# Kernel tuning notes

Hardware: AMD Instinct MI355X
Metric: run time of the kernel (lower is better)

Reference implementation:

```python
import jax, jax.numpy as jnp
import numpy as np
from jax import lax

B, T, C, H, N = 4, 1024, 2048, 32, 64
KVH = 8            # kv heads -> kv_dim = 512, n_rep = 4
GN_EPS = 0.00064   # group_norm eps from Step3


def _l2norm(x):
    # torch F.normalize(p=2, dim=-1) with eps=1e-12
    n = jnp.linalg.norm(x, axis=-1, keepdims=True)
    return x / jnp.maximum(n, 1e-12)


def _rwkv7_scan(r, decay, k, v, aa, bb, state):
    # all inputs (B,T,H,N); state (B,H,N,N) with layout [value, key]
    def step(S, inp):
        r_t, d_t, k_t, v_t, a_t, b_t = inp  # each (B,H,N)
        sa = jnp.einsum('bhik,bhk->bhi', S, a_t)
        S = (S * d_t[:, :, None, :]
             + sa[..., None] * b_t[:, :, None, :]
             + v_t[..., None] * k_t[:, :, None, :])
        y = jnp.einsum('bhik,bhk->bhi', S, r_t)
        return S, y
    xs = tuple(jnp.moveaxis(t, 1, 0) for t in (r, decay, k, v, aa, bb))  # (T,B,H,N)
    state, ys = lax.scan(step, state, xs)
    return jnp.moveaxis(ys, 0, 1), state  # (B,T,H,N), (B,H,N,N)


def _forward(x, v_first, state, R, R_bias, K, K_bias, V, V_bias, O, O_bias,
             w0, w1, w2, a0, a1, a2, v0, v1, v2, k_k, k_a, r_k, ln_w, ln_b):
    # ---- Step1: projections + gates (hybrid_matmul -> plain matmul in fp32 ref) ----
    r = x @ R.T + R_bias                                   # (B,T,C)
    w_raw = -jax.nn.softplus(-(w0 + jnp.tanh(x @ w1) @ w2)) - 0.6
    k = x @ K.T + K_bias                                   # (B,T,512)
    v = x @ V.T + V_bias
    n_rep = C // K.shape[0]
    k = jnp.repeat(k.reshape(B, T, KVH, N), n_rep, axis=2).reshape(B, T, C)
    v = jnp.repeat(v.reshape(B, T, KVH, N), n_rep, axis=2).reshape(B, T, C)
    a = jax.nn.sigmoid(a0 + (x @ a1) @ a2)
    kk = _l2norm((k * k_k).reshape(B, T, H, N)).reshape(B, T, C)
    k = k * (1.0 + (a - 1.0) * k_a)
    # layer_id != 0: cross-layer value blending
    v = v + (v_first - v) * jax.nn.sigmoid(v0 + (x @ v1) @ v2)
    aa = -kk
    bb = kk * a
    # ---- Step2: fused recurrent rwkv7 (fp32 state) ----
    decay = jnp.exp(-jnp.exp(w_raw.astype(jnp.float32)))
    rs = lambda t: t.astype(jnp.float32).reshape(B, T, H, N)
    y, state_out = _rwkv7_scan(rs(r), decay.reshape(B, T, H, N), rs(k), rs(v), rs(aa), rs(bb), state)
    # ---- Step3: group norm over (T, N) per (batch, head) as in the (B,C,T) permute ----
    mean = y.mean(axis=(1, 3), keepdims=True)
    var = ((y - mean) ** 2).mean(axis=(1, 3), keepdims=True)
    yn = (y - mean) * lax.rsqrt(var + GN_EPS)
    xx = (yn * ln_w.reshape(H, N) + ln_b.reshape(H, N)).reshape(B, T, C)
    bonus = ((r.reshape(B, T, H, N) * k.reshape(B, T, H, N) * r_k.reshape(H, N))
             .sum(-1, keepdims=True) * v.reshape(B, T, H, N)).reshape(B, T, C)
    xx = xx + bonus
    out = xx @ O.T + O_bias
    return out


def setup_inputs() -> dict:
    key = jax.random.key(0)
    ks = jax.random.split(key, 25)
    g = lambda i, shape, s: jax.random.normal(ks[i], shape, dtype=jnp.float32) * s
    return {
        'x': g(0, (B, T, C), 1.0),
        'v_first': g(1, (B, T, C), 1.0),
        'state': jnp.zeros((B, H, N, N), dtype=jnp.float32),
        'R': g(2, (C, C), 0.02), 'R_bias': jnp.zeros((C,), jnp.float32),
        'K': g(3, (KVH * N, C), 0.02), 'K_bias': jnp.zeros((KVH * N,), jnp.float32),
        'V': g(4, (KVH * N, C), 0.02), 'V_bias': jnp.zeros((KVH * N,), jnp.float32),
        'O': g(5, (C, C), 0.02), 'O_bias': jnp.zeros((C,), jnp.float32),
        'w0': g(6, (C,), 0.1), 'w1': g(7, (C, 64), 0.05), 'w2': g(8, (64, C), 0.05),
        'a0': g(9, (C,), 0.1), 'a1': g(10, (C, 64), 0.05), 'a2': g(11, (64, C), 0.05),
        'v0': g(12, (C,), 0.1), 'v1': g(13, (C, 32), 0.05), 'v2': g(14, (32, C), 0.05),
        'k_k': 1.0 + g(15, (C,), 0.05),
        'k_a': 1.0 + g(16, (C,), 0.05),
        'r_k': g(17, (C,), 0.1),
        'ln_w': jnp.ones((C,), jnp.float32),
        'ln_b': jnp.zeros((C,), jnp.float32),
    }


def reference(x, v_first, state, R, R_bias, K, K_bias, V, V_bias, O, O_bias,
              w0, w1, w2, a0, a1, a2, v0, v1, v2, k_k, k_a, r_k, ln_w, ln_b):
    return _forward(x, v_first, state, R, R_bias, K, K_bias, V, V_bias, O, O_bias,
                    w0, w1, w2, a0, a1, a2, v0, v1, v2, k_k, k_a, r_k, ln_w, ln_b)
```

## Files before the change

### kernel.cpp

```cpp
#include <hip/hip_runtime.h>
#include <hip/hip_bf16.h>
#include <math.h>

typedef __attribute__((ext_vector_type(8))) short bf16x8;
typedef __attribute__((ext_vector_type(4))) float f32x4;

__device__ __forceinline__ unsigned short f2b(float f) {
  unsigned u = __float_as_uint(f);
  unsigned r = (u + 0x7FFF + ((u >> 16) & 1)) >> 16;
  return (unsigned short)r;
}

__device__ __forceinline__ void async16(const void* g, void* l) {
  __builtin_amdgcn_global_load_lds(
      (const __attribute__((address_space(1))) unsigned int*)(g),
      (__attribute__((address_space(3))) unsigned int*)(l), 16, 0, 0);
}

__device__ __forceinline__ float rowsum16(float x) {
  x += __int_as_float(__builtin_amdgcn_update_dpp(0, __float_as_int(x), 0x121, 0xF, 0xF, false));
  x += __int_as_float(__builtin_amdgcn_update_dpp(0, __float_as_int(x), 0x122, 0xF, 0xF, false));
  x += __int_as_float(__builtin_amdgcn_update_dpp(0, __float_as_int(x), 0x124, 0xF, 0xF, false));
  x += __int_as_float(__builtin_amdgcn_update_dpp(0, __float_as_int(x), 0x128, 0xF, 0xF, false));
  return x;
}

__device__ __forceinline__ float mixhi(float a, unsigned pk, float c) {
  float d;
  asm("v_fma_mix_f32 %0, %1, %2, %3 op_sel:[0,1,0] op_sel_hi:[0,1,0]"
      : "=v"(d) : "v"(a), "v"(pk), "v"(c));
  return d;
}
__device__ __forceinline__ float mixlo(float a, unsigned pk, float c) {
  float d;
  asm("v_fma_mix_f32 %0, %1, %2, %3 op_sel:[0,0,0] op_sel_hi:[0,1,0]"
      : "=v"(d) : "v"(a), "v"(pk), "v"(c));
  return d;
}
__device__ __forceinline__ float h2f(unsigned h) {
  float f; asm("v_cvt_f32_f16 %0, %1" : "=v"(f) : "v"(h)); return f;
}

__global__ __launch_bounds__(256) void cvt4_kernel(
    const float* __restrict__ x, const float* __restrict__ R,
    const float* __restrict__ K, const float* __restrict__ V,
    const float* __restrict__ Ow,
    unsigned short* __restrict__ xb, unsigned short* __restrict__ RKVb,
    unsigned short* __restrict__ Ob)
{
  const int bid = blockIdx.x;
  const float* s; unsigned short* d; int i;
  if (bid < 8192)       { s = x; d = xb; i = bid * 256 + threadIdx.x; }
  else if (bid < 12288) { s = R; d = RKVb; i = (bid - 8192) * 256 + threadIdx.x; }
  else if (bid < 13312) { s = K; d = RKVb + 2048 * 2048; i = (bid - 12288) * 256 + threadIdx.x; }
  else if (bid < 14336) { s = V; d = RKVb + 2560 * 2048; i = (bid - 13312) * 256 + threadIdx.x; }
  else                  { s = Ow; d = Ob; i = (bid - 14336) * 256 + threadIdx.x; }
  float4 v = ((const float4*)s)[i];
  ushort4 o;
  o.x = f2b(v.x); o.y = f2b(v.y); o.z = f2b(v.z); o.w = f2b(v.w);
  ((ushort4*)d)[i] = o;
}

__global__ __launch_bounds__(256) void tcvt_all(
    const float* __restrict__ w1, const float* __restrict__ a1,
    const float* __restrict__ v1, const float* __restrict__ w2,
    const float* __restrict__ a2, const float* __restrict__ v2,
    unsigned short* __restrict__ Bcat, unsigned short* __restrict__ w2t,
    unsigned short* __restrict__ a2t, unsigned short* __restrict__ v2t)
{
  const int r = blockIdx.x >> 5, i = blockIdx.x & 31;
  const float* in; unsigned short* out; int Kd, Nd, ors, bx, by;
  switch (r) {
    case 0:  in = w1; out = Bcat;             Kd = 2048; Nd = 64;   ors = 2048; bx = 0; by = i; break;
    case 1:  in = a1; out = Bcat + 64 * 2048; Kd = 2048; Nd = 64;   ors = 2048; bx = 0; by = i; break;
    case 2:  in = v1; out = Bcat + 128 * 2048; Kd = 2048; Nd = 32;  ors = 2048; bx = 0; by = i; break;
    case 3:  in = w2; out = w2t;              Kd = 64;   Nd = 2048; ors = 64;   bx = i; by = 0; break;
    case 4:  in = a2; out = a2t;              Kd = 64;   Nd = 2048; ors = 64;   bx = i; by = 0; break;
    default: in = v2; out = v2t;              Kd = 32;   Nd = 2048; ors = 32;   bx = i; by = 0; break;
  }
  __shared__ unsigned short tile[64][65];
  const int tx = threadIdx.x & 63, ty = threadIdx.x >> 6;
  const int n0 = bx * 64, k0 = by * 64;
  #pragma unroll
  for (int j = 0; j < 16; ++j) {
    const int k = k0 + j * 4 + ty;
    const int n = n0 + tx;
    unsigned short v = 0;
    if (k < Kd && n < Nd) v = f2b(in[(size_t)k * Nd + n]);
    tile[j * 4 + ty][tx] = v;
  }
  __syncthreads();
  #pragma unroll
  for (int j = 0; j < 16; ++j) {
    const int n = n0 + j * 4 + ty;
    const int k = k0 + tx;
    if (n < Nd && k < Kd) out[(size_t)n * ors + k] = tile[tx][j * 4 + ty];
  }
}

template<int OUTBF16, int ACT>
__device__ __forceinline__ void gemm_body(
    const unsigned short* __restrict__ A, int lda,
    const unsigned short* __restrict__ B, int ldb,
    const float* __restrict__ bias, void* __restrict__ Cv, int ldc,
    int M, int N, int K, int row0, int col0)
{
  __shared__ __align__(16) unsigned short As[128 * 32];
  __shared__ __align__(16) unsigned short Bs[128 * 32];
  const int tid = threadIdx.x;
  const int w = tid >> 6, lane = tid & 63;
  const int wr = (w >> 1) * 64, wc = (w & 1) * 64;

  f32x4 acc[4][4];
  #pragma unroll
  for (int i = 0; i < 4; ++i)
    #pragma unroll
    for (int j = 0; j < 4; ++j)
      acc[i][j] = (f32x4){0.f, 0.f, 0.f, 0.f};

  const int srow = w * 32 + (lane >> 2);
  const int scol = (lane & 3) * 8;
  const int brow0 = (col0 + srow < N) ? (col0 + srow) : 0;
  const int brow1 = (col0 + srow + 16 < N) ? (col0 + srow + 16) : 0;
  const unsigned short* gA0 = A + (size_t)(row0 + srow) * lda + scol;
  const unsigned short* gA1 = gA0 + (size_t)16 * lda;
  const unsigned short* gB0 = B + (size_t)brow0 * ldb + scol;
  const unsigned short* gB1 = B + (size_t)brow1 * ldb + scol;
  unsigned short* lA0 = As + w * 1024;
  unsigned short* lA1 = As + w * 1024 + 512;
  unsigned short* lB0 = Bs + w * 1024;
  unsigned short* lB1 = Bs + w * 1024 + 512;

  const int m16 = lane & 15;
  const int q8  = (lane >> 4) * 8;

  for (int k0 = 0; k0 < K; k0 += 32) {
    async16(gA0, lA0);
    async16(gA1, lA1);
    async16(gB0, lB0);
    async16(gB1, lB1);
    gA0 += 32; gA1 += 32; gB0 += 32; gB1 += 32;
    __syncthreads();
    bf16x8 af[4], bfr[4];
    #pragma unroll
    for (int i = 0; i < 4; ++i) {
      af[i]  = *(const bf16x8*)(As + (wr + i * 16 + m16) * 32 + q8);
      bfr[i] = *(const bf16x8*)(Bs + (wc + i * 16 + m16) * 32 + q8);
    }
    #pragma unroll
    for (int i = 0; i < 4; ++i)
      #pragma unroll
      for (int j = 0; j < 4; ++j)
        acc[i][j] = __builtin_amdgcn_mfma_f32_16x16x32_bf16(af[i], bfr[j], acc[i][j], 0, 0, 0);
    __syncthreads();
  }

  #pragma unroll
  for (int j = 0; j < 4; ++j) {
    const int c_ = col0 + wc + j * 16 + (lane & 15);
    if (c_ < N) {
      const float bv = bias ? bias[c_] : 0.f;
      #pragma unroll
      for (int i = 0; i < 4; ++i) {
        const int r_ = row0 + wr + i * 16 + (lane >> 4) * 4;
        #pragma unroll
        for (int t4 = 0; t4 < 4; ++t4) {
          float v = acc[i][j][t4] + bv;
          if (ACT == 2 && c_ < 64) v = tanhf(v);
          if (OUTBF16)
            ((unsigned short*)Cv)[(size_t)(r_ + t4) * ldc + c_] = f2b(v);
          else
            ((float*)Cv)[(size_t)(r_ + t4) * ldc + c_] = v;
        }
      }
    }
  }
}

template<int OUTBF16, int ACT>
__global__ __launch_bounds__(256) void gemm_mfma(
    const unsigned short* __restrict__ A, int lda,
    const unsigned short* __restrict__ B, int ldb,
    const float* __restrict__ bias, void* __restrict__ Cv, int ldc,
    int M, int N, int K)
{
  gemm_body<OUTBF16, ACT>(A, lda, B, ldb, bias, Cv, ldc, M, N, K,
                          blockIdx.y * 128, blockIdx.x * 128);
}

__global__ __launch_bounds__(256) void gemm_lr2(
    const unsigned short* __restrict__ hcat,
    const unsigned short* __restrict__ w2t,
    const unsigned short* __restrict__ a2t,
    const unsigned short* __restrict__ v2t,
    float* __restrict__ wt, float* __restrict__ at, float* __restrict__ vt)
{
  const int z = blockIdx.z;
  const unsigned short* A; const unsigned short* Bm; float* C; int K;
  if (z == 0)      { A = hcat;       Bm = w2t; C = wt; K = 64; }
  else if (z == 1) { A = hcat + 64;  Bm = a2t; C = at; K = 64; }
  else             { A = hcat + 128; Bm = v2t; C = vt; K = 32; }
  gemm_body<0, 0>(A, 160, Bm, K, nullptr, C, 2048, 4096, 2048, K,
                  blockIdx.y * 128, blockIdx.x * 128);
}

__global__ __launch_bounds__(256) void gemm_rkvh(
    const unsigned short* __restrict__ A, const unsigned short* __restrict__ B,
    const float* __restrict__ Rb_, const float* __restrict__ Kb_,
    const float* __restrict__ Vb_,
    float* __restrict__ Cr, float* __restrict__ Ck, float* __restrict__ Cvv,
    unsigned short* __restrict__ hcat)
{
  const int col0 = blockIdx.x * 128;
  const int row0 = blockIdx.y * 128;
  float* Cf = nullptr; unsigned short* Ch = nullptr;
  int ldc, cbase; const float* bias = nullptr;
  if (col0 < 2048)      { Cf = Cr;  ldc = 2048; cbase = col0;        bias = Rb_; }
  else if (col0 < 2560) { Cf = Ck;  ldc = 512;  cbase = col0 - 2048; bias = Kb_; }
  else if (col0 < 3072) { Cf = Cvv; ldc = 512;  cbase = col0 - 2560; bias = Vb_; }
  else                  { Ch = hcat; ldc = 160; cbase = col0 - 3072; }

  __shared__ __align__(16) unsigned short As[128 * 32];
  __shared__ __align__(16) unsigned short Bs[128 * 32];
  const int tid = threadIdx.x;
  const int w = tid >> 6, lane = tid & 63;
  const int wr = (w >> 1) * 64, wc = (w & 1) * 64;

  f32x4 acc[4][4];
  #pragma unroll
  for (int i = 0; i < 4; ++i)
    #pragma unroll
    for (int j = 0; j < 4; ++j)
      acc[i][j] = (f32x4){0.f, 0.f, 0.f, 0.f};

  const int srow = w * 32 + (lane >> 2);
  const int scol = (lane & 3) * 8;
  const int brow0 = (col0 + srow < 3232) ? (col0 + srow) : 0;
  const int brow1 = (col0 + srow + 16 < 3232) ? (col0 + srow + 16) : 0;
  const unsigned short* gA0 = A + (size_t)(row0 + srow) * 2048 + scol;
  const unsigned short* gA1 = gA0 + (size_t)16 * 2048;
  const unsigned short* gB0 = B + (size_t)brow0 * 2048 + scol;
  const unsigned short* gB1 = B + (size_t)brow1 * 2048 + scol;
  unsigned short* lA0 = As + w * 1024;
  unsigned short* lA1 = As + w * 1024 + 512;
  unsigned short* lB0 = Bs + w * 1024;
  unsigned short* lB1 = Bs + w * 1024 + 512;

  const int m16 = lane & 15;
  const int q8  = (lane >> 4) * 8;

  for (int k0 = 0; k0 < 2048; k0 += 32) {
    async16(gA0, lA0);
    async16(gA1, lA1);
    async16(gB0, lB0);
    async16(gB1, lB1);
    gA0 += 32; gA1 += 32; gB0 += 32; gB1 += 32;
    __syncthreads();
    bf16x8 af[4], bfr[4];
    #pragma unroll
    for (int i = 0; i < 4; ++i) {
      af[i]  = *(const bf16x8*)(As + (wr + i * 16 + m16) * 32 + q8);
      bfr[i] = *(const bf16x8*)(Bs + (wc + i * 16 + m16) * 32 + q8);
    }
    #pragma unroll
    for (int i = 0; i < 4; ++i)
      #pragma unroll
      for (int j = 0; j < 4; ++j)
        acc[i][j] = __builtin_amdgcn_mfma_f32_16x16x32_bf16(af[i], bfr[j], acc[i][j], 0, 0, 0);
    __syncthreads();
  }

  #pragma unroll
  for (int j = 0; j < 4; ++j) {
    const int c_ = cbase + wc + j * 16 + (lane & 15);
    if (Ch) {
      if (c_ < 160) {
        #pragma unroll
        for (int i = 0; i < 4; ++i) {
          const int r_ = row0 + wr + i * 16 + (lane >> 4) * 4;
          #pragma unroll
          for (int t4 = 0; t4 < 4; ++t4) {
            float v = acc[i][j][t4];
            if (c_ < 64) v = tanhf(v);
            Ch[(size_t)(r_ + t4) * 160 + c_] = f2b(v);
          }
        }
      }
    } else {
      const float bv = bias[c_];
      #pragma unroll
      for (int i = 0; i < 4; ++i) {
        const int r_ = row0 + wr + i * 16 + (lane >> 4) * 4;
        #pragma unroll
        for (int t4 = 0; t4 < 4; ++t4)
          Cf[(size_t)(r_ + t4) * ldc + c_] = acc[i][j][t4] + bv;
      }
    }
  }
}

__global__ __launch_bounds__(256) void prep_kernel(
    const float* __restrict__ k_buf, const float* __restrict__ v_buf,
    const float* __restrict__ r_buf,
    float* wt_decay, const float* __restrict__ at, float* vt_vf,
    const float* __restrict__ v_first,
    const float* __restrict__ w0, const float* __restrict__ a0,
    const float* __restrict__ v0, const float* __restrict__ k_k,
    const float* __restrict__ k_a,
    unsigned* __restrict__ rk_pk, unsigned* __restrict__ ab_pk)
{
  const int row = blockIdx.x;
  const int tid = threadIdx.x;
  const int c0 = tid << 3;
  const int h = tid >> 3;
  const int kvoff = (h >> 2) << 6;
  const size_t base = (size_t)row * 2048;
  const size_t kvrow = (size_t)row * 512;
  float kr[8], kkr[8];
  float ss = 0.f;
  #pragma unroll
  for (int e = 0; e < 8; ++e) {
    const int c = c0 + e;
    const float kv = k_buf[kvrow + kvoff + (c & 63)];
    kr[e] = kv;
    const float t = kv * k_k[c];
    kkr[e] = t;
    ss = fmaf(t, t, ss);
  }
  ss += __shfl_xor(ss, 1);
  ss += __shfl_xor(ss, 2);
  ss += __shfl_xor(ss, 4);
  const float inv = 1.f / fmaxf(sqrtf(ss), 1e-12f);
  #pragma unroll
  for (int e = 0; e < 8; ++e) {
    const int c = c0 + e;
    const size_t idx = base + c;
    const float kk = kkr[e] * inv;
    const float a = 1.f / (1.f + expf(-(a0[c] + at[idx])));
    const float u = w0[c] + wt_decay[idx];
    const float sig_u = 1.f / (1.f + expf(-u));
    wt_decay[idx] = expf(-0.5488116360940264f * sig_u);
    const float kfin = kr[e] * fmaf(a - 1.f, k_a[c], 1.f);
    const float vr = v_buf[kvrow + kvoff + (c & 63)];
    const float sv = 1.f / (1.f + expf(-(v0[c] + vt_vf[idx])));
    vt_vf[idx] = vr + (v_first[idx] - vr) * sv;
    const float bbv = kk * a;
    const float aav = -kk;
    unsigned rk_u, ab_u;
    asm("v_cvt_pkrtz_f16_f32 %0, %1, %2" : "=v"(rk_u) : "v"(r_buf[idx]), "v"(kfin));
    asm("v_cvt_pkrtz_f16_f32 %0, %1, %2" : "=v"(ab_u) : "v"(bbv), "v"(aav));
    rk_pk[idx] = rk_u;
    ab_pk[idx] = ab_u;
  }
}

#define WB(n) asm volatile("s_waitcnt vmcnt(" #n ") lgkmcnt(0)\n\ts_barrier" ::: "memory")
#define BAR2() asm volatile("s_waitcnt lgkmcnt(0)\n\ts_barrier" ::: "memory")

__global__ __launch_bounds__(256) void scan_kernel(
    const unsigned* __restrict__ rkB, const unsigned* __restrict__ abB,
    const float* __restrict__ dB, const float* __restrict__ vB,
    const float* __restrict__ state, float* __restrict__ y,
    float* __restrict__ part)
{
  __shared__ float lds[13824];
  unsigned* ldsU = (unsigned*)lds;
  const int tid = threadIdx.x;
  const int bid = blockIdx.x;
  const int xcd = bid & 7, bj = bid >> 3;
  const int m = bj & 3, gq = bj >> 2;
  const int bh = (gq << 3) | xcd;
  const int widx = tid >> 6;
  const int lane = tid & 63;
  const int rg = lane >> 4;
  const int colg = lane & 15;
  const int rowb = (widx << 2) + rg;
  const int row = (m << 4) + rowb;
  const int b = bh >> 5, h = bh & 31;

  float4 S = *(const float4*)(state + (size_t)bh * 4096 + row * 64 + (colg << 2));

  const unsigned cb = (unsigned)((b * 1024) * 2048 + h * 64);
  const unsigned srow8 = (unsigned)((widx << 3) + rg);
  const unsigned scol = (unsigned)(colg << 2);
  const unsigned sseg = (unsigned)(widx << 9);

  float sacc = 0.f, ssacc = 0.f;
  const float fzero = 0.0f;

  #define STAGE(step0, bofs) do {                                            \
    const unsigned go0_ = cb + ((step0) + srow8) * 2048u + scol;             \
    const unsigned go1_ = go0_ + 4u * 2048u;                                 \
    async16(rkB + go0_, ldsU + (bofs) + sseg);                               \
    async16(rkB + go1_, ldsU + (bofs) + sseg + 256);                         \
    async16(abB + go0_, ldsU + (bofs) + 2048 + sseg);                        \
    async16(abB + go1_, ldsU + (bofs) + 2048 + sseg + 256);                  \
    async16(dB + go0_,  lds + (bofs) + 4096 + sseg);                         \
    async16(dB + go1_,  lds + (bofs) + 4096 + sseg + 256);                   \
    if (lane < 32) {                                                         \
      const unsigned gv_ = cb + ((step0) + (unsigned)(widx << 3)             \
                                 + (unsigned)(lane >> 2)) * 2048u            \
                           + (unsigned)(m << 4) + (unsigned)((lane & 3) << 2); \
      async16(vB + gv_, lds + (bofs) + 6144 + (widx << 7));                  \
    }                                                                        \
  } while (0)

  #define LDRK(bofs, s) (*(const uint4*)(ldsU + (bofs) + (s) * 64 + (colg << 2)))
  #define LDAB(bofs, s) (*(const uint4*)(ldsU + (bofs) + 2048 + (s) * 64 + (colg << 2)))
  #define LDD(bofs, s)  (*(const float4*)(lds + (bofs) + 4096 + (s) * 64 + (colg << 2)))
  #define LDV(bofs, s)  (lds[(bofs) + 6144 + ((s) << 4) + rowb])

  #define PROCESS(bofs) do {                                                 \
    uint4 rk0 = LDRK(bofs, 0), ab0 = LDAB(bofs, 0);                          \
    float4 dv0 = LDD(bofs, 0); float vv0 = LDV(bofs, 0);                     \
    uint4 rk1 = LDRK(bofs, 1), ab1 = LDAB(bofs, 1);                          \
    float4 dv1 = LDD(bofs, 1); float vv1 = LDV(bofs, 1);                     \
    _Pragma("unroll")                                                        \
    for (int s = 0; s < 32; ++s) {                                           \
      const bool ev = ((s & 1) == 0);                                        \
      const uint4 rkc = ev ? rk0 : rk1;                                      \
      const uint4 abc = ev ? ab0 : ab1;                                      \
      const float4 dvc = ev ? dv0 : dv1;                                     \
      const float vvc = ev ? vv0 : vv1;                                      \
      if (s < 30) {                                                          \
        if (ev) {                                                            \
          rk0 = LDRK(bofs, s + 2); ab0 = LDAB(bofs, s + 2);                  \
          dv0 = LDD(bofs, s + 2);  vv0 = LDV(bofs, s + 2);                   \
        } else {                                                             \
          rk1 = LDRK(bofs, s + 2); ab1 = LDAB(bofs, s + 2);                  \
          dv1 = LDD(bofs, s + 2);  vv1 = LDV(bofs, s + 2);                   \
        }                                                                    \
      }                                                                      \
      float t0 = mixhi(S.x, abc.x, fzero);                                   \
      t0 = mixhi(S.y, abc.y, t0);                                            \
      t0 = mixhi(S.z, abc.z, t0);                                            \
      t0 = mixhi(S.w, abc.w, t0);                                            \
      const float sa = rowsum16(t0);                                         \
      float p0 = mixhi(vvc, rkc.x, fzero);                                   \
      float p1 = mixhi(vvc, rkc.y, fzero);                                   \
      float p2 = mixhi(vvc, rkc.z, fzero);                                   \
      float p3 = mixhi(vvc, rkc.w, fzero);                                   \
      p0 = mixlo(sa, abc.x, p0);                                             \
      p1 = mixlo(sa, abc.y, p1);                                             \
      p2 = mixlo(sa, abc.z, p2);                                             \
      p3 = mixlo(sa, abc.w, p3);                                             \
      S.x = fmaf(S.x, dvc.x, p0);                                            \
      S.y = fmaf(S.y, dvc.y, p1);                                            \
      S.z = fmaf(S.z, dvc.z, p2);                                            \
      S.w = fmaf(S.w, dvc.w, p3);                                            \
      float t1 = mixlo(S.x, rkc.x, fzero);                                   \
      t1 = mixlo(S.y, rkc.y, t1);                                            \
      t1 = mixlo(S.z, rkc.z, t1);                                            \
      t1 = mixlo(S.w, rkc.w, t1);                                            \
      const float yv = rowsum16(t1);                                         \
      if (colg == 0) {                                                       \
        lds[13312 + (s << 4) + rowb] = yv;                                   \
        sacc += yv;                                                          \
        ssacc = fmaf(yv, yv, ssacc);                                         \
      }                                                                      \
    }                                                                        \
  } while (0)

  #define YSTORE(step0) do {                                                 \
    const float y0_ = lds[13312 + tid];                                      \
    const float y1_ = lds[13312 + 256 + tid];                                \
    y[cb + ((step0) + (unsigned)(tid >> 4)) * 2048u +                        \
      (unsigned)(m << 4) + (unsigned)(tid & 15)] = y0_;                      \
    y[cb + ((step0) + 16u + (unsigned)(tid >> 4)) * 2048u +                  \
      (unsigned)(m << 4) + (unsigned)(tid & 15)] = y1_;                      \
  } while (0)

  STAGE(0u, 0);
  STAGE(32u, 6656);

  WB(7);
  PROCESS(0);
  BAR2();
  YSTORE(0u);
  STAGE(64u, 0);

  for (int c = 1; c <= 30; ++c) {
    const int bofs = (c & 1) ? 6656 : 0;
    WB(9);
    PROCESS(bofs);
    BAR2();
    YSTORE((unsigned)(c << 5));
    if (c < 30) STAGE((unsigned)((c + 2) << 5), bofs);
  }

  WB(2);
  PROCESS(6656);
  BAR2();
  YSTORE(992u);

  sacc  += __shfl_xor(sacc, 16);
  sacc  += __shfl_xor(sacc, 32);
  ssacc += __shfl_xor(ssacc, 16);
  ssacc += __shfl_xor(ssacc, 32);
  __syncthreads();
  if (lane == 0) { lds[widx] = sacc; lds[4 + widx] = ssacc; }
  __syncthreads();
  if (tid == 0) {
    const float s_  = lds[0] + lds[1] + lds[2] + lds[3];
    const float ss_ = lds[4] + lds[5] + lds[6] + lds[7];
    ((float2*)part)[(bh << 2) + m] = make_float2(s_, ss_);
  }

  #undef STAGE
  #undef PROCESS
  #undef YSTORE
  #undef LDRK
  #undef LDAB
  #undef LDD
  #undef LDV
}

__global__ __launch_bounds__(256) void gapply_kernel(
    const float* __restrict__ y, const unsigned* __restrict__ rkB,
    const float* __restrict__ vf,
    const float* __restrict__ part, const float* __restrict__ r_k,
    const float* __restrict__ ln_w, const float* __restrict__ ln_b,
    unsigned short* __restrict__ xxb)
{
  const int row = blockIdx.x;
  const int b = row >> 10;
  const int tid = threadIdx.x;
  const int h = tid >> 3;
  const int bh = b * 32 + h;
  float s = 0.f, ss = 0.f;
  #pragma unroll
  for (int j = 0; j < 4; ++j) {
    const float2 pr = ((const float2*)part)[(bh << 2) + j];
    s += pr.x; ss += pr.y;
  }
  const float mean = s * (1.f / 65536.f);
  const float rstd = rsqrtf(ss * (1.f / 65536.f) - mean * mean + 0.00064f);
  const int c0 = tid << 3;
  const size_t base = (size_t)row * 2048 + c0;
  float yv[8], vv[8];
  float p = 0.f;
  #pragma unroll
  for (int e = 0; e < 8; ++e) {
    yv[e] = y[base + e];
    vv[e] = vf[base + e];
    const unsigned w_ = rkB[base + e];
    p = fmaf(h2f(w_ & 0xffffu) * h2f(w_ >> 16), r_k[c0 + e], p);
  }
  p += __shfl_xor(p, 1);
  p += __shfl_xor(p, 2);
  p += __shfl_xor(p, 4);
  #pragma unroll
  for (int e = 0; e < 8; ++e) {
    const float yn = (yv[e] - mean) * rstd;
    xxb[base + e] = f2b(fmaf(yn, ln_w[c0 + e], ln_b[c0 + e]) + p * vv[e]);
  }
}

extern "C" void kernel_launch(void* const* d_in, const int* in_sizes, int n_in,
                              void* d_out, int out_size, void* d_ws, size_t ws_size,
                              hipStream_t stream) {
  const float* x       = (const float*)d_in[0];
  const float* v_first = (const float*)d_in[1];
  const float* state   = (const float*)d_in[2];
  const float* Rw      = (const float*)d_in[3];
  const float* R_bias  = (const float*)d_in[4];
  const float* Kw      = (const float*)d_in[5];
  const float* K_bias  = (const float*)d_in[6];
  const float* Vw      = (const float*)d_in[7];
  const float* V_bias  = (const float*)d_in[8];
  const float* Ow      = (const float*)d_in[9];
  const float* O_bias  = (const float*)d_in[10];
  const float* w0      = (const float*)d_in[11];
  const float* w1      = (const float*)d_in[12];
  const float* w2      = (const float*)d_in[13];
  const float* a0      = (const float*)d_in[14];
  const float* a1      = (const float*)d_in[15];
  const float* a2      = (const float*)d_in[16];
  const float* v0      = (const float*)d_in[17];
  const float* v1      = (const float*)d_in[18];
  const float* v2      = (const float*)d_in[19];
  const float* k_k     = (const float*)d_in[20];
  const float* k_a     = (const float*)d_in[21];
  const float* r_k     = (const float*)d_in[22];
  const float* ln_w    = (const float*)d_in[23];
  const float* ln_b    = (const float*)d_in[24];

  float* ws = (float*)d_ws;
  float* r_buf = ws;
  float* k_buf = r_buf + 8388608;
  float* v_buf = k_buf + 2097152;
  float* wt    = v_buf + 2097152;
  float* at    = wt    + 8388608;
  float* vt    = at    + 8388608;
  float* kf    = vt    + 8388608;
  float* aaq   = kf    + 8388608;
  float* bbq   = aaq   + 8388608;
  float* part  = bbq   + 8388608;
  unsigned short* xb   = (unsigned short*)bbq;
  unsigned short* RKVb = (unsigned short*)kf;
  unsigned short* Bcat = RKVb + 3072 * 2048;
  unsigned short* hcat = (unsigned short*)(kf + 3400000);
  unsigned short* w2t  = (unsigned short*)(kf + 3800000);
  unsigned short* a2t  = (unsigned short*)(kf + 3900000);
  unsigned short* v2t  = (unsigned short*)(kf + 4000000);
  unsigned short* Ob   = (unsigned short*)(kf + 4500000);
  unsigned* rk_pk      = (unsigned*)aaq;
  unsigned* ab_pk      = (unsigned*)bbq;
  unsigned short* xxb  = (unsigned short*)bbq;

  dim3 blk(256);
  cvt4_kernel<<<18432, blk, 0, stream>>>(x, Rw, Kw, Vw, Ow, xb, RKVb, Ob);
  tcvt_all<<<192, blk, 0, stream>>>(w1, a1, v1, w2, a2, v2, Bcat, w2t, a2t, v2t);
  gemm_rkvh<<<dim3(26, 32), blk, 0, stream>>>(xb, RKVb, R_bias, K_bias, V_bias,
                                              r_buf, k_buf, v_buf, hcat);
  gemm_lr2<<<dim3(16, 32, 3), blk, 0, stream>>>(hcat, w2t, a2t, v2t, wt, at, vt);
  prep_kernel<<<4096, blk, 0, stream>>>(k_buf, v_buf, r_buf, wt, at, vt, v_first,
                                        w0, a0, v0, k_k, k_a, rk_pk, ab_pk);
  float* ybuf = at;
  scan_kernel<<<512, blk, 0, stream>>>(rk_pk, ab_pk, wt, vt, state, ybuf, part);
  gapply_kernel<<<4096, blk, 0, stream>>>(ybuf, rk_pk, vt, part, r_k,
                                          ln_w, ln_b, xxb);
  gemm_mfma<0,0><<<dim3(16, 32), blk, 0, stream>>>(xxb, 2048, Ob, 2048, O_bias,
                                                   (float*)d_out, 2048, 4096, 2048, 2048);
}
```

Measured before the change: 724.6 us.

## Give each scan thread two state rows and remap GEMM blocks across XCDs

The scan kernel now splits each (batch, head) state over two blocks instead of four. Each thread holds two state rows, so every loaded r/k/a/b/decay vector is reused twice, the redundant per-block staging of shared inputs is halved and y is written with float4 stores. The grid shrinks from 512 to 256 blocks, which lowers parallelism and adds register pressure. The RKV and output GEMMs also use a 1-D grid with an XCD-aware block swizzle so neighbouring tiles land on the same XCD's L2.

Result: slower. 750.1 us (+3.5%).

```diff
diff --git a/kernel.cpp b/kernel.cpp
--- a/kernel.cpp
+++ b/kernel.cpp
@@ -177,15 +177,15 @@
   }
 }
 
-template<int OUTBF16, int ACT>
-__global__ __launch_bounds__(256) void gemm_mfma(
-    const unsigned short* __restrict__ A, int lda,
-    const unsigned short* __restrict__ B, int ldb,
-    const float* __restrict__ bias, void* __restrict__ Cv, int ldc,
-    int M, int N, int K)
-{
-  gemm_body<OUTBF16, ACT>(A, lda, B, ldb, bias, Cv, ldc, M, N, K,
-                          blockIdx.y * 128, blockIdx.x * 128);
+__global__ __launch_bounds__(256) void gemm_out(
+    const unsigned short* __restrict__ A,
+    const unsigned short* __restrict__ B,
+    const float* __restrict__ bias, float* __restrict__ C)
+{
+  const int lb = (blockIdx.x & 7) * 64 + (blockIdx.x >> 3);
+  const int bx = lb & 15, by = lb >> 4;
+  gemm_body<0, 0>(A, 2048, B, 2048, bias, C, 2048, 4096, 2048, 2048,
+                  by * 128, bx * 128);
 }
 
 __global__ __launch_bounds__(256) void gemm_lr2(
@@ -211,8 +211,9 @@
     float* __restrict__ Cr, float* __restrict__ Ck, float* __restrict__ Cvv,
     unsigned short* __restrict__ hcat)
 {
-  const int col0 = blockIdx.x * 128;
-  const int row0 = blockIdx.y * 128;
+  const int lb = (blockIdx.x & 7) * 104 + (blockIdx.x >> 3);
+  const int col0 = (lb % 26) * 128;
+  const int row0 = (lb / 26) * 128;
   float* Cf = nullptr; unsigned short* Ch = nullptr;
   int ldc, cbase; const float* bias = nullptr;
   if (col0 < 2048)      { Cf = Cr;  ldc = 2048; cbase = col0;        bias = Rb_; }
@@ -363,65 +364,116 @@
     const float* __restrict__ state, float* __restrict__ y,
     float* __restrict__ part)
 {
-  __shared__ float lds[13824];
+  __shared__ float lds[15360];
   unsigned* ldsU = (unsigned*)lds;
   const int tid = threadIdx.x;
   const int bid = blockIdx.x;
   const int xcd = bid & 7, bj = bid >> 3;
-  const int m = bj & 3, gq = bj >> 2;
-  const int bh = (gq << 3) | xcd;
+  const int half = bj & 1, bhq = bj >> 1;
+  const int bh = (bhq << 3) | xcd;
   const int widx = tid >> 6;
   const int lane = tid & 63;
   const int rg = lane >> 4;
   const int colg = lane & 15;
-  const int rowb = (widx << 2) + rg;
-  const int row = (m << 4) + rowb;
+  const int r0b = (widx << 3) + (rg << 1);
+  const int row = (half << 5) + r0b;
   const int b = bh >> 5, h = bh & 31;
 
-  float4 S = *(const float4*)(state + (size_t)bh * 4096 + row * 64 + (colg << 2));
+  float4 S0 = *(const float4*)(state + (size_t)bh * 4096 + row * 64 + (colg << 2));
+  float4 S1 = *(const float4*)(state + (size_t)bh * 4096 + (row + 1) * 64 + (colg << 2));
 
   const unsigned cb = (unsigned)((b * 1024) * 2048 + h * 64);
-  const unsigned srow8 = (unsigned)((widx << 3) + rg);
-  const unsigned scol = (unsigned)(colg << 2);
-  const unsigned sseg = (unsigned)(widx << 9);
+  const unsigned sstep = (unsigned)(tid >> 4);
+  const unsigned scol  = (unsigned)((tid & 15) << 2);
+  const unsigned vstep = (unsigned)(tid >> 3);
+  const unsigned vcol  = (unsigned)((tid & 7) << 2);
 
   float sacc = 0.f, ssacc = 0.f;
   const float fzero = 0.0f;
 
   #define STAGE(step0, bofs) do {                                            \
-    const unsigned go0_ = cb + ((step0) + srow8) * 2048u + scol;             \
-    const unsigned go1_ = go0_ + 4u * 2048u;                                 \
-    async16(rkB + go0_, ldsU + (bofs) + sseg);                               \
-    async16(rkB + go1_, ldsU + (bofs) + sseg + 256);                         \
-    async16(abB + go0_, ldsU + (bofs) + 2048 + sseg);                        \
-    async16(abB + go1_, ldsU + (bofs) + 2048 + sseg + 256);                  \
-    async16(dB + go0_,  lds + (bofs) + 4096 + sseg);                         \
-    async16(dB + go1_,  lds + (bofs) + 4096 + sseg + 256);                   \
-    if (lane < 32) {                                                         \
-      const unsigned gv_ = cb + ((step0) + (unsigned)(widx << 3)             \
-                                 + (unsigned)(lane >> 2)) * 2048u            \
-                           + (unsigned)(m << 4) + (unsigned)((lane & 3) << 2); \
-      async16(vB + gv_, lds + (bofs) + 6144 + (widx << 7));                  \
-    }                                                                        \
+    const unsigned g0_ = cb + ((step0) + sstep) * 2048u + scol;              \
+    const unsigned g1_ = g0_ + 16u * 2048u;                                  \
+    async16(rkB + g0_, ldsU + (bofs) + tid * 4);                             \
+    async16(rkB + g1_, ldsU + (bofs) + 1024 + tid * 4);                      \
+    async16(abB + g0_, ldsU + (bofs) + 2048 + tid * 4);                      \
+    async16(abB + g1_, ldsU + (bofs) + 3072 + tid * 4);                      \
+    async16(dB + g0_,  lds + (bofs) + 4096 + tid * 4);                       \
+    async16(dB + g1_,  lds + (bofs) + 5120 + tid * 4);                       \
+    const unsigned gv_ = cb + ((step0) + vstep) * 2048u                      \
+                         + (unsigned)(half << 5) + vcol;                     \
+    async16(vB + gv_, lds + (bofs) + 6144 + tid * 4);                        \
   } while (0)
 
   #define LDRK(bofs, s) (*(const uint4*)(ldsU + (bofs) + (s) * 64 + (colg << 2)))
   #define LDAB(bofs, s) (*(const uint4*)(ldsU + (bofs) + 2048 + (s) * 64 + (colg << 2)))
   #define LDD(bofs, s)  (*(const float4*)(lds + (bofs) + 4096 + (s) * 64 + (colg << 2)))
-  #define LDV(bofs, s)  (lds[(bofs) + 6144 + ((s) << 4) + rowb])
+  #define LDV(bofs, s)  (*(const float2*)(lds + (bofs) + 6144 + (s) * 32 + r0b))
+
+  #define STEPBODY(rkc, abc, dvc, vvc, s) do {                               \
+    float t0a = mixhi(S0.x, abc.x, fzero);                                   \
+    t0a = mixhi(S0.y, abc.y, t0a);                                           \
+    t0a = mixhi(S0.z, abc.z, t0a);                                           \
+    t0a = mixhi(S0.w, abc.w, t0a);                                           \
+    float t0b = mixhi(S1.x, abc.x, fzero);                                   \
+    t0b = mixhi(S1.y, abc.y, t0b);                                           \
+    t0b = mixhi(S1.z, abc.z, t0b);                                           \
+    t0b = mixhi(S1.w, abc.w, t0b);                                           \
+    const float sa0 = rowsum16(t0a);                                         \
+    const float sa1 = rowsum16(t0b);                                         \
+    float p00 = mixhi(vvc.x, rkc.x, fzero);                                  \
+    float p01 = mixhi(vvc.x, rkc.y, fzero);                                  \
+    float p02 = mixhi(vvc.x, rkc.z, fzero);                                  \
+    float p03 = mixhi(vvc.x, rkc.w, fzero);                                  \
+    float p10 = mixhi(vvc.y, rkc.x, fzero);                                  \
+    float p11 = mixhi(vvc.y, rkc.y, fzero);                                  \
+    float p12 = mixhi(vvc.y, rkc.z, fzero);                                  \
+    float p13 = mixhi(vvc.y, rkc.w, fzero);                                  \
+    p00 = mixlo(sa0, abc.x, p00);                                            \
+    p01 = mixlo(sa0, abc.y, p01);                                            \
+    p02 = mixlo(sa0, abc.z, p02);                                            \
+    p03 = mixlo(sa0, abc.w, p03);                                            \
+    p10 = mixlo(sa1, abc.x, p10);                                            \
+    p11 = mixlo(sa1, abc.y, p11);                                            \
+    p12 = mixlo(sa1, abc.z, p12);                                            \
+    p13 = mixlo(sa1, abc.w, p13);                                            \
+    S0.x = fmaf(S0.x, dvc.x, p00);                                           \
+    S0.y = fmaf(S0.y, dvc.y, p01);                                           \
+    S0.z = fmaf(S0.z, dvc.z, p02);                                           \
+    S0.w = fmaf(S0.w, dvc.w, p03);                                           \
+    S1.x = fmaf(S1.x, dvc.x, p10);                                           \
+    S1.y = fmaf(S1.y, dvc.y, p11);                                           \
+    S1.z = fmaf(S1.z, dvc.z, p12);                                           \
+    S1.w = fmaf(S1.w, dvc.w, p13);                                           \
+    float t1a = mixlo(S0.x, rkc.x, fzero);                                   \
+    t1a = mixlo(S0.y, rkc.y, t1a);                                           \
+    t1a = mixlo(S0.z, rkc.z, t1a);                                           \
+    t1a = mixlo(S0.w, rkc.w, t1a);                                           \
+    float t1b = mixlo(S1.x, rkc.x, fzero);                                   \
+    t1b = mixlo(S1.y, rkc.y, t1b);                                           \
+    t1b = mixlo(S1.z, rkc.z, t1b);                                           \
+    t1b = mixlo(S1.w, rkc.w, t1b);                                           \
+    const float y0 = rowsum16(t1a);                                          \
+    const float y1 = rowsum16(t1b);                                          \
+    if (colg == 0) {                                                         \
+      *(float2*)(lds + 14336 + ((s) << 5) + r0b) = make_float2(y0, y1);      \
+      sacc += y0 + y1;                                                       \
+      ssacc = fmaf(y0, y0, fmaf(y1, y1, ssacc));                             \
+    }                                                                        \
+  } while (0)
 
   #define PROCESS(bofs) do {                                                 \
     uint4 rk0 = LDRK(bofs, 0), ab0 = LDAB(bofs, 0);                          \
-    float4 dv0 = LDD(bofs, 0); float vv0 = LDV(bofs, 0);                     \
+    float4 dv0 = LDD(bofs, 0); float2 vv0 = LDV(bofs, 0);                    \
     uint4 rk1 = LDRK(bofs, 1), ab1 = LDAB(bofs, 1);                          \
-    float4 dv1 = LDD(bofs, 1); float vv1 = LDV(bofs, 1);                     \
+    float4 dv1 = LDD(bofs, 1); float2 vv1 = LDV(bofs, 1);                    \
     _Pragma("unroll")                                                        \
     for (int s = 0; s < 32; ++s) {                                           \
       const bool ev = ((s & 1) == 0);                                        \
       const uint4 rkc = ev ? rk0 : rk1;                                      \
       const uint4 abc = ev ? ab0 : ab1;                                      \
       const float4 dvc = ev ? dv0 : dv1;                                     \
-      const float vvc = ev ? vv0 : vv1;                                      \
+      const float2 vvc = ev ? vv0 : vv1;                                     \
       if (s < 30) {                                                          \
         if (ev) {                                                            \
           rk0 = LDRK(bofs, s + 2); ab0 = LDAB(bofs, s + 2);                  \
@@ -431,47 +483,18 @@
           dv1 = LDD(bofs, s + 2);  vv1 = LDV(bofs, s + 2);                   \
         }                                                                    \
       }                                                                      \
-      float t0 = mixhi(S.x, abc.x, fzero);                                   \
-      t0 = mixhi(S.y, abc.y, t0);                                            \
-      t0 = mixhi(S.z, abc.z, t0);                                            \
-      t0 = mixhi(S.w, abc.w, t0);                                            \
-      const float sa = rowsum16(t0);                                         \
-      float p0 = mixhi(vvc, rkc.x, fzero);                                   \
-      float p1 = mixhi(vvc, rkc.y, fzero);                                   \
-      float p2 = mixhi(vvc, rkc.z, fzero);                                   \
-      float p3 = mixhi(vvc, rkc.w, fzero);                                   \
-      p0 = mixlo(sa, abc.x, p0);                                             \
-      p1 = mixlo(sa, abc.y, p1);                                             \
-      p2 = mixlo(sa, abc.z, p2);                                             \
-      p3 = mixlo(sa, abc.w, p3);                                             \
-      S.x = fmaf(S.x, dvc.x, p0);                                            \
-      S.y = fmaf(S.y, dvc.y, p1);                                            \
-      S.z = fmaf(S.z, dvc.z, p2);                                            \
-      S.w = fmaf(S.w, dvc.w, p3);                                            \
-      float t1 = mixlo(S.x, rkc.x, fzero);                                   \
-      t1 = mixlo(S.y, rkc.y, t1);                                            \
-      t1 = mixlo(S.z, rkc.z, t1);                                            \
-      t1 = mixlo(S.w, rkc.w, t1);                                            \
-      const float yv = rowsum16(t1);                                         \
-      if (colg == 0) {                                                       \
-        lds[13312 + (s << 4) + rowb] = yv;                                   \
-        sacc += yv;                                                          \
-        ssacc = fmaf(yv, yv, ssacc);                                         \
-      }                                                                      \
+      STEPBODY(rkc, abc, dvc, vvc, s);                                       \
     }                                                                        \
   } while (0)
 
   #define YSTORE(step0) do {                                                 \
-    const float y0_ = lds[13312 + tid];                                      \
-    const float y1_ = lds[13312 + 256 + tid];                                \
-    y[cb + ((step0) + (unsigned)(tid >> 4)) * 2048u +                        \
-      (unsigned)(m << 4) + (unsigned)(tid & 15)] = y0_;                      \
-    y[cb + ((step0) + 16u + (unsigned)(tid >> 4)) * 2048u +                  \
-      (unsigned)(m << 4) + (unsigned)(tid & 15)] = y1_;                      \
+    const float4 yv_ = *(const float4*)(lds + 14336 + tid * 4);              \
+    *(float4*)(y + cb + ((step0) + vstep) * 2048u                            \
+               + (unsigned)(half << 5) + vcol) = yv_;                        \
   } while (0)
 
   STAGE(0u, 0);
-  STAGE(32u, 6656);
+  STAGE(32u, 7168);
 
   WB(7);
   PROCESS(0);
@@ -480,16 +503,16 @@
   STAGE(64u, 0);
 
   for (int c = 1; c <= 30; ++c) {
-    const int bofs = (c & 1) ? 6656 : 0;
-    WB(9);
+    const int bofs = (c & 1) ? 7168 : 0;
+    WB(8);
     PROCESS(bofs);
     BAR2();
     YSTORE((unsigned)(c << 5));
     if (c < 30) STAGE((unsigned)((c + 2) << 5), bofs);
   }
 
-  WB(2);
-  PROCESS(6656);
+  WB(1);
+  PROCESS(7168);
   BAR2();
   YSTORE(992u);
 
@@ -503,11 +526,12 @@
   if (tid == 0) {
     const float s_  = lds[0] + lds[1] + lds[2] + lds[3];
     const float ss_ = lds[4] + lds[5] + lds[6] + lds[7];
-    ((float2*)part)[(bh << 2) + m] = make_float2(s_, ss_);
+    ((float2*)part)[(bh << 1) + half] = make_float2(s_, ss_);
   }
 
   #undef STAGE
   #undef PROCESS
+  #undef STEPBODY
   #undef YSTORE
   #undef LDRK
   #undef LDAB
@@ -529,8 +553,8 @@
   const int bh = b * 32 + h;
   float s = 0.f, ss = 0.f;
   #pragma unroll
-  for (int j = 0; j < 4; ++j) {
-    const float2 pr = ((const float2*)part)[(bh << 2) + j];
+  for (int j = 0; j < 2; ++j) {
+    const float2 pr = ((const float2*)part)[(bh << 1) + j];
     s += pr.x; ss += pr.y;
   }
   const float mean = s * (1.f / 65536.f);
@@ -611,15 +635,14 @@
   dim3 blk(256);
   cvt4_kernel<<<18432, blk, 0, stream>>>(x, Rw, Kw, Vw, Ow, xb, RKVb, Ob);
   tcvt_all<<<192, blk, 0, stream>>>(w1, a1, v1, w2, a2, v2, Bcat, w2t, a2t, v2t);
-  gemm_rkvh<<<dim3(26, 32), blk, 0, stream>>>(xb, RKVb, R_bias, K_bias, V_bias,
-                                              r_buf, k_buf, v_buf, hcat);
+  gemm_rkvh<<<832, blk, 0, stream>>>(xb, RKVb, R_bias, K_bias, V_bias,
+                                     r_buf, k_buf, v_buf, hcat);
   gemm_lr2<<<dim3(16, 32, 3), blk, 0, stream>>>(hcat, w2t, a2t, v2t, wt, at, vt);
   prep_kernel<<<4096, blk, 0, stream>>>(k_buf, v_buf, r_buf, wt, at, vt, v_first,
                                         w0, a0, v0, k_k, k_a, rk_pk, ab_pk);
   float* ybuf = at;
-  scan_kernel<<<512, blk, 0, stream>>>(rk_pk, ab_pk, wt, vt, state, ybuf, part);
+  scan_kernel<<<256, blk, 0, stream>>>(rk_pk, ab_pk, wt, vt, state, ybuf, part);
   gapply_kernel<<<4096, blk, 0, stream>>>(ybuf, rk_pk, vt, part, r_k,
                                           ln_w, ln_b, xxb);
-  gemm_mfma<0,0><<<dim3(16, 32), blk, 0, stream>>>(xxb, 2048, Ob, 2048, O_bias,
-                                                   (float*)d_out, 2048, 4096, 2048, 2048);
-}
+  gemm_out<<<512, blk, 0, stream>>>(xxb, Ob, O_bias, (float*)d_out);
+}
```
